# Kernel optimization log

Measured on AMD Instinct MI355X. Metric: run time of the kernel, lower is better.

## Reference

```python
import math
import jax, jax.numpy as jnp
from jax import lax
import numpy as np

D_MODEL, D_STATE, D_CONV, EXPAND = 96, 16, 3, 2
D_INNER = EXPAND * D_MODEL            # 192
DT_RANK = math.ceil(D_MODEL / 16)     # 6
B_, H_, W_ = 2, 64, 64


def setup_inputs() -> dict:
    key = jax.random.key(0)
    ks = jax.random.split(key, 8)
    x = jax.random.normal(ks[0], (B_, H_, W_, D_MODEL), jnp.float32)
    in_proj_w = jax.random.normal(ks[1], (2 * D_INNER, D_MODEL), jnp.float32) * (D_MODEL ** -0.5)
    conv_w = jax.random.normal(ks[2], (D_INNER, 1, D_CONV, D_CONV), jnp.float32) * 0.1  # depthwise OIHW
    conv_b = jax.random.normal(ks[3], (D_INNER,), jnp.float32) * 0.1
    x_proj_weight = jax.random.normal(ks[4], (4, DT_RANK + 2 * D_STATE, D_INNER), jnp.float32) * (D_INNER ** -0.5)
    dt_init_std = DT_RANK ** -0.5
    dt_projs_weight = jax.random.uniform(ks[5], (4, D_INNER, DT_RANK), jnp.float32, -dt_init_std, dt_init_std)
    dt = jnp.exp(jax.random.uniform(ks[6], (4, D_INNER), jnp.float32) * (math.log(0.1) - math.log(0.001)) + math.log(0.001))
    dt = jnp.clip(dt, 1e-4, None)
    dt_projs_bias = dt + jnp.log(-jnp.expm1(-dt))  # inverse softplus init
    A_logs = jnp.log(jnp.tile(jnp.arange(1.0, D_STATE + 1.0, dtype=jnp.float32), (4 * D_INNER, 1)))  # (4*D, N)
    Ds = jnp.ones((4 * D_INNER,), jnp.float32)
    out_norm_w = jnp.ones((D_INNER,), jnp.float32)
    out_norm_b = jnp.zeros((D_INNER,), jnp.float32)
    out_proj_w = jax.random.normal(ks[7], (D_MODEL, D_INNER), jnp.float32) * (D_INNER ** -0.5)
    return dict(x=x, in_proj_w=in_proj_w, conv_w=conv_w, conv_b=conv_b,
                x_proj_weight=x_proj_weight, dt_projs_weight=dt_projs_weight,
                dt_projs_bias=dt_projs_bias, A_logs=A_logs, Ds=Ds,
                out_norm_w=out_norm_w, out_norm_b=out_norm_b, out_proj_w=out_proj_w)


def _ss2d(x, in_proj_w, conv_w, conv_b, x_proj_weight, dt_projs_weight,
          dt_projs_bias, A_logs, Ds, out_norm_w, out_norm_b, out_proj_w):
    B, H, W, C = x.shape
    K = 4
    d_inner = conv_w.shape[0]
    d_state = A_logs.shape[1]
    dt_rank = dt_projs_weight.shape[2]
    L = H * W

    # in_proj + split into x / gate z
    xz = jnp.einsum('bhwc,ec->bhwe', x, in_proj_w)
    xi, z = jnp.split(xz, 2, axis=-1)

    # depthwise 3x3 conv (padding=1) + SiLU, channels-first
    xc = jnp.transpose(xi, (0, 3, 1, 2))  # B,D,H,W
    xc = lax.conv_general_dilated(xc, conv_w, (1, 1), 'SAME',
                                  feature_group_count=d_inner,
                                  dimension_numbers=('NCHW', 'OIHW', 'NCHW'))
    xc = jax.nn.silu(xc + conv_b[None, :, None, None])

    # 4 scan directions: row-major, col-major, and their reverses
    x_hw = xc.reshape(B, d_inner, L)
    x_wh = jnp.transpose(xc, (0, 1, 3, 2)).reshape(B, d_inner, L)
    x_hwwh = jnp.stack([x_hw, x_wh], axis=1)                        # B,2,D,L
    xs = jnp.concatenate([x_hwwh, jnp.flip(x_hwwh, axis=-1)], axis=1)  # B,K,D,L

    x_dbl = jnp.einsum('bkdl,kcd->bkcl', xs, x_proj_weight)
    dts, Bs, Cs = jnp.split(x_dbl, [dt_rank, dt_rank + d_state], axis=2)
    dts = jnp.einsum('bkrl,kdr->bkdl', dts, dt_projs_weight)
    delta = jax.nn.softplus(dts + dt_projs_bias[None, :, :, None])  # B,K,D,L
    A = -jnp.exp(A_logs).reshape(K, d_inner, d_state)               # K,D,N

    # selective scan over L (serial recurrence)
    d_s = jnp.moveaxis(delta, -1, 0)  # L,B,K,D
    u_s = jnp.moveaxis(xs, -1, 0)     # L,B,K,D
    B_s = jnp.moveaxis(Bs, -1, 0)     # L,B,K,N
    C_s = jnp.moveaxis(Cs, -1, 0)     # L,B,K,N

    def step(h, inp):
        d_t, u_t, Bt, Ct = inp
        dA = jnp.exp(d_t[..., None] * A)                       # B,K,D,N
        h = h * dA + (d_t * u_t)[..., None] * Bt[:, :, None, :]
        y = jnp.einsum('bkdn,bkn->bkd', h, Ct)
        return h, y

    h0 = jnp.zeros((B, K, d_inner, d_state), jnp.float32)
    _, ys = lax.scan(step, h0, (d_s, u_s, B_s, C_s))  # ys: L,B,K,D
    ys = jnp.moveaxis(ys, 0, -1)                      # B,K,D,L
    out_y = ys + xs * Ds.reshape(K, d_inner)[None, :, :, None]

    # merge directions back to row-major layout
    inv_y = jnp.flip(out_y[:, 2:4], axis=-1)
    wh_y = jnp.transpose(out_y[:, 1].reshape(B, d_inner, W, H), (0, 1, 3, 2)).reshape(B, d_inner, L)
    invwh_y = jnp.transpose(inv_y[:, 1].reshape(B, d_inner, W, H), (0, 1, 3, 2)).reshape(B, d_inner, L)
    y = out_y[:, 0] + inv_y[:, 0] + wh_y + invwh_y    # B,D,L

    y = jnp.transpose(y, (0, 2, 1)).reshape(B, H, W, d_inner)
    mu = y.mean(-1, keepdims=True)
    var = y.var(-1, keepdims=True)
    y = (y - mu) * lax.rsqrt(var + 1e-5) * out_norm_w + out_norm_b
    y = y * jax.nn.silu(z)
    return jnp.einsum('bhwd,cd->bhwc', y, out_proj_w)


def reference(x, in_proj_w, conv_w, conv_b, x_proj_weight, dt_projs_weight,
              dt_projs_bias, A_logs, Ds, out_norm_w, out_norm_b, out_proj_w):
    return _ss2d(x, in_proj_w, conv_w, conv_b, x_proj_weight, dt_projs_weight,
                 dt_projs_bias, A_logs, Ds, out_norm_w, out_norm_b, out_proj_w)
```

## Files before the change

### kernel.cpp

```cpp
#include <hip/hip_runtime.h>
#include <math.h>

#define DMODEL 96
#define DIN    192
#define NST    16
#define RK     6
#define KDIR   4
#define LLEN   4096
#define BB     2
#define BP_TOT 8192
#define SCH    128
#define TCH    32

typedef float v2f __attribute__((ext_vector_type(2)));

#if __has_builtin(__builtin_elementwise_fma)
__device__ __forceinline__ v2f pk_fma(v2f a, v2f b, v2f c) { return __builtin_elementwise_fma(a, b, c); }
#else
__device__ __forceinline__ v2f pk_fma(v2f a, v2f b, v2f c) { return a * b + c; }
#endif

__global__ __launch_bounds__(192) void k_inproj(const float* __restrict__ x,
                                                const float* __restrict__ Wp,
                                                float* __restrict__ xi,
                                                float* __restrict__ z)
{
    __shared__ float xs[8 * 96];
    const int t  = threadIdx.x;
    const int p0 = blockIdx.x * 8;
    for (int idx = t; idx < 768; idx += 192)
        xs[idx] = x[(size_t)p0 * 96 + idx];
    __syncthreads();

    float acc0[8], acc1[8];
    #pragma unroll
    for (int i = 0; i < 8; ++i) { acc0[i] = 0.f; acc1[i] = 0.f; }
    const float* w0p = Wp + (size_t)t * 96;
    const float* w1p = Wp + (size_t)(t + 192) * 96;
    for (int k = 0; k < 96; k += 4) {
        float4 w0 = *(const float4*)(w0p + k);
        float4 w1 = *(const float4*)(w1p + k);
        #pragma unroll
        for (int p = 0; p < 8; ++p) {
            float4 xv = *(const float4*)&xs[p * 96 + k];
            acc0[p] = fmaf(w0.x, xv.x, fmaf(w0.y, xv.y, fmaf(w0.z, xv.z, fmaf(w0.w, xv.w, acc0[p]))));
            acc1[p] = fmaf(w1.x, xv.x, fmaf(w1.y, xv.y, fmaf(w1.z, xv.z, fmaf(w1.w, xv.w, acc1[p]))));
        }
    }
    #pragma unroll
    for (int p = 0; p < 8; ++p) {
        xi[(size_t)(p0 + p) * 192 + t] = acc0[p];
        z [(size_t)(p0 + p) * 192 + t] = acc1[p];
    }
}

__device__ __forceinline__ int inv_perm(int kd, int p)
{
    if (kd == 0) return p;
    if (kd == 1) return ((p & 63) << 6) | (p >> 6);
    if (kd == 2) return 4095 - p;
    return 4095 - (((p & 63) << 6) | (p >> 6));
}

__device__ __forceinline__ int perm_pos(int k, int l)
{
    if (k == 0) return l;
    if (k == 1) return ((l & 63) << 6) | (l >> 6);
    if (k == 2) return 4095 - l;
    int lr = 4095 - l;
    return ((lr & 63) << 6) | (lr >> 6);
}

__device__ __forceinline__ int perm_dir(int k)
{
    return (k == 0) ? 1 : (k == 1) ? 64 : (k == 2) ? -1 : -64;
}

__device__ __forceinline__ float softplus_fast(float x)
{
    float r = __logf(1.f + __expf(x));
    return (x > 15.f) ? x : r;
}

__device__ __forceinline__ void pow_chain_pk(float e1, v2f* aa)
{
    float e2 = e1 * e1;
    v2f a0; a0.x = e1; a0.y = e2;
    v2f s2; s2.x = e2; s2.y = e2;
    v2f a1 = a0 * s2;
    float e4 = a1.y;
    v2f s4; s4.x = e4; s4.y = e4;
    v2f a2 = a0 * s4;
    v2f a3 = a1 * s4;
    float e8 = a3.y;
    v2f s8; s8.x = e8; s8.y = e8;
    aa[0] = a0; aa[1] = a1; aa[2] = a2; aa[3] = a3;
    aa[4] = a0 * s8;
    aa[5] = a1 * s8;
    aa[6] = a2 * s8;
    aa[7] = a3 * s8;
}

__device__ __forceinline__ float pow_n(float W, int e)
{
    float w2 = W * W, w4 = w2 * w2, w8 = w4 * w4;
    float r = 1.f;
    if (e & 1) r *= W;
    if (e & 2) r *= w2;
    if (e & 4) r *= w4;
    if (e & 8) r *= w8;
    if (e & 16) r = w8 * w8;
    return r;
}

__device__ __forceinline__ int sm_remap(int c)
{
    return (c < 6) ? (32 + c) : (c - 6);
}

__global__ __launch_bounds__(192) void k_convxdbl(const float* __restrict__ xi,
                                                  const float* __restrict__ cw,
                                                  const float* __restrict__ cb,
                                                  const float* __restrict__ xpw,
                                                  float* __restrict__ xc,
                                                  float* __restrict__ xdk)
{
    __shared__ float xs[8 * 192];
    const int t   = threadIdx.x;
    const int p0  = blockIdx.x * 8;
    const int b   = p0 >> 12;
    const int pp0 = p0 & 4095;
    const int row = pp0 >> 6, c0 = pp0 & 63;

    float w9[9];
    #pragma unroll
    for (int i = 0; i < 9; ++i) w9[i] = cw[t * 9 + i];
    const float cbias = cb[t];

    float xv[3][10];
    #pragma unroll
    for (int ky = 0; ky < 3; ++ky) {
        int rr = row + ky - 1;
        #pragma unroll
        for (int kx = 0; kx < 10; ++kx) {
            int cc = c0 + kx - 1;
            float v = 0.f;
            if (rr >= 0 && rr < 64 && cc >= 0 && cc < 64)
                v = xi[((size_t)b * 4096 + rr * 64 + cc) * 192 + t];
            xv[ky][kx] = v;
        }
    }
    #pragma unroll
    for (int p = 0; p < 8; ++p) {
        float s = cbias;
        #pragma unroll
        for (int ky = 0; ky < 3; ++ky)
            #pragma unroll
            for (int kx = 0; kx < 3; ++kx)
                s = fmaf(xv[ky][p + kx], w9[ky * 3 + kx], s);
        float sv = s * (1.f / (1.f + __expf(-s)));
        xc[(size_t)(p0 + p) * 192 + t] = sv;
        xs[p * 192 + t] = sv;
    }
    __syncthreads();
    if (t >= 152) return;

    const int kd = t / 38, r = t % 38;
    float acc[8];
    #pragma unroll
    for (int i = 0; i < 8; ++i) acc[i] = 0.f;
    const float* wr = xpw + (size_t)t * 192;
    for (int k = 0; k < 192; k += 4) {
        float4 w = *(const float4*)(wr + k);
        #pragma unroll
        for (int p = 0; p < 8; ++p) {
            float4 x4 = *(const float4*)&xs[p * 192 + k];
            acc[p] = fmaf(w.x, x4.x, fmaf(w.y, x4.y, fmaf(w.z, x4.z, fmaf(w.w, x4.w, acc[p]))));
        }
    }
    #pragma unroll
    for (int p = 0; p < 8; ++p) {
        int pp = pp0 + p;
        int l  = inv_perm(kd, pp);
        xdk[((size_t)(b * 4 + kd) * 4096 + l) * 38 + r] = acc[p];
    }
}

__global__ __launch_bounds__(192) void k_scan1(const float* __restrict__ xc,
                                               const float* __restrict__ xdk,
                                               const float* __restrict__ dtw,
                                               const float* __restrict__ dtb,
                                               const float* __restrict__ Alog,
                                               float* __restrict__ hend,
                                               float* __restrict__ prodA,
                                               float* __restrict__ Wbuf)
{
    __shared__ float sm[TCH * 40];
    __shared__ float su[TCH * 192];
    const int t   = threadIdx.x;
    const int blk = blockIdx.x;
    const int s = blk & (SCH - 1), k = (blk >> 7) & 3, b = blk >> 9;
    const int kd = k * 192 + t;
    const int l0 = s * TCH;
    const int pstart = perm_pos(k, l0);
    const int dir    = perm_dir(k);

    const float* src = xdk + ((size_t)(b * 4 + k) * 4096 + l0) * 38;
    for (int idx = t; idx < TCH * 38; idx += 192) {
        int st = idx / 38, c = idx % 38;
        sm[st * 40 + sm_remap(c)] = src[idx];
    }
    const float* xcb = xc + (size_t)b * 4096 * 192;
    #pragma unroll
    for (int i = 0; i < TCH; ++i)
        su[i * 192 + t] = xcb[(size_t)(pstart + i * dir) * 192 + t];

    const float A0 = -__expf(Alog[kd * 16]);
    bool fast = true;
    #pragma unroll
    for (int n = 1; n < 16; ++n) {
        float An = -__expf(Alog[kd * 16 + n]);
        fast = fast && (fabsf(An - (float)(n + 1) * A0) <= 1e-3f * fabsf(An));
    }
    float wdt[6];
    #pragma unroll
    for (int r = 0; r < 6; ++r) wdt[r] = dtw[kd * 6 + r];
    const float bias = dtb[kd];

    __syncthreads();

    size_t base = (size_t)blk * 3072 + t * 16;

    if (fast) {
        v2f h2[8];
        #pragma unroll
        for (int i = 0; i < 8; ++i) { h2[i].x = 0.f; h2[i].y = 0.f; }
        float cd = 0.f;
        for (int st = 0; st < TCH; ++st) {
            const float* r = &sm[st * 40];
            float u = su[st * 192 + t];
            float4 dq = *(const float4*)(r + 32);
            float xv = bias + dq.x * wdt[0] + dq.y * wdt[1] + dq.z * wdt[2]
                            + dq.w * wdt[3] + r[36] * wdt[4] + r[37] * wdt[5];
            float delta = softplus_fast(xv);
            cd += delta;
            float du = delta * u;
            v2f du2; du2.x = du; du2.y = du;
            v2f aa2[8];
            pow_chain_pk(__expf(delta * A0), aa2);
            const v2f* rb = (const v2f*)r;
            #pragma unroll
            for (int i = 0; i < 8; ++i)
                h2[i] = pk_fma(h2[i], aa2[i], du2 * rb[i]);
        }
        Wbuf[(size_t)blk * 192 + t] = __expf(cd * A0);
        #pragma unroll
        for (int i = 0; i < 4; ++i)
            *(float4*)&hend[base + 4 * i] =
                make_float4(h2[2*i].x, h2[2*i].y, h2[2*i+1].x, h2[2*i+1].y);
    } else {
        float h[16];
        #pragma unroll
        for (int n = 0; n < 16; ++n) h[n] = 0.f;
        float cd = 0.f;
        for (int st = 0; st < TCH; ++st) {
            const float* r = &sm[st * 40];
            float u = su[st * 192 + t];
            float xv = bias;
            #pragma unroll
            for (int j = 0; j < 6; ++j) xv += r[32 + j] * wdt[j];
            float delta = softplus_fast(xv);
            cd += delta;
            float du = delta * u;
            #pragma unroll
            for (int n = 0; n < 16; ++n) {
                float An = -__expf(Alog[kd * 16 + n]);
                h[n] = fmaf(h[n], __expf(delta * An), du * r[n]);
            }
        }
        #pragma unroll
        for (int n = 0; n < 16; ++n)
            prodA[base + n] = __expf(-__expf(Alog[kd * 16 + n]) * cd);
        #pragma unroll
        for (int i = 0; i < 4; ++i)
            *(float4*)&hend[base + 4 * i] = make_float4(h[4*i], h[4*i+1], h[4*i+2], h[4*i+3]);
    }
}

__global__ __launch_bounds__(256) void k_scan2(const float* __restrict__ hend,
                                               float* __restrict__ prodA,
                                               const float* __restrict__ Wbuf,
                                               const float* __restrict__ Alog)
{
    __shared__ float smA[256], smH[256];
    const int t = threadIdx.x;
    const int g = t >> 4, n = t & 15;
    const int bk = blockIdx.x / 192, d = blockIdx.x % 192;
    const int kd = (bk & 3) * 192 + d;
    const size_t base = (size_t)bk * SCH * 3072 + d * 16 + n;

    const float A0 = -__expf(Alog[kd * 16]);
    bool fast = true;
    #pragma unroll
    for (int m = 1; m < 16; ++m) {
        float An = -__expf(Alog[kd * 16 + m]);
        fast = fast && (fabsf(An - (float)(m + 1) * A0) <= 1e-3f * fabsf(An));
    }

    float a_[8], h_[8];
    float A = 1.f, H = 0.f;
    #pragma unroll
    for (int i = 0; i < 8; ++i) {
        int s = g * 8 + i;
        size_t rec = base + (size_t)s * 3072;
        float ai;
        if (fast) {
            float W = Wbuf[((size_t)bk * SCH + s) * 192 + d];
            ai = pow_n(W, n + 1);
        } else {
            ai = prodA[rec];
        }
        a_[i] = ai;
        h_[i] = hend[rec];
        H = fmaf(ai, H, h_[i]);
        A *= ai;
    }
    smA[t] = A; smH[t] = H;
    __syncthreads();
    if (t < 16) {
        float carry = 0.f;
        for (int g2 = 0; g2 < 16; ++g2) {
            float ta = smA[g2 * 16 + t], th = smH[g2 * 16 + t];
            smH[g2 * 16 + t] = carry;
            carry = fmaf(ta, carry, th);
        }
    }
    __syncthreads();
    float carry = smH[t];
    #pragma unroll
    for (int i = 0; i < 8; ++i) {
        size_t rec = base + (size_t)(g * 8 + i) * 3072;
        prodA[rec] = carry;
        carry = fmaf(a_[i], carry, h_[i]);
    }
}

__global__ __launch_bounds__(192) void k_scan3(const float* __restrict__ xc,
                                               const float* __restrict__ xdk,
                                               const float* __restrict__ dtw,
                                               const float* __restrict__ dtb,
                                               const float* __restrict__ Alog,
                                               const float* __restrict__ Ds,
                                               const float* __restrict__ hinit,
                                               float* __restrict__ yk)
{
    __shared__ float sm[TCH * 40];
    __shared__ float su[TCH * 192];
    const int t   = threadIdx.x;
    const int blk = blockIdx.x;
    const int s = blk & (SCH - 1), k = (blk >> 7) & 3, b = blk >> 9;
    const int kd = k * 192 + t;
    const int l0 = s * TCH;
    const int pstart = perm_pos(k, l0);
    const int dir    = perm_dir(k);

    const float* src = xdk + ((size_t)(b * 4 + k) * 4096 + l0) * 38;
    for (int idx = t; idx < TCH * 38; idx += 192) {
        int st = idx / 38, c = idx % 38;
        sm[st * 40 + sm_remap(c)] = src[idx];
    }
    const float* xcb = xc + (size_t)b * 4096 * 192;
    #pragma unroll
    for (int i = 0; i < TCH; ++i)
        su[i * 192 + t] = xcb[(size_t)(pstart + i * dir) * 192 + t];

    const float A0 = -__expf(Alog[kd * 16]);
    bool fast = true;
    #pragma unroll
    for (int n = 1; n < 16; ++n) {
        float An = -__expf(Alog[kd * 16 + n]);
        fast = fast && (fabsf(An - (float)(n + 1) * A0) <= 1e-3f * fabsf(An));
    }
    float wdt[6];
    #pragma unroll
    for (int r = 0; r < 6; ++r) wdt[r] = dtw[kd * 6 + r];
    const float bias = dtb[kd];
    const float Dk   = Ds[kd];

    size_t hbase = (size_t)blk * 3072 + t * 16;
    float* yp = yk + (size_t)(b * 4 + k) * 4096 * 192 + (size_t)pstart * 192 + t;
    const int ystep = dir * 192;

    __syncthreads();

    if (fast) {
        v2f h2[8];
        #pragma unroll
        for (int i = 0; i < 4; ++i) {
            float4 v = *(const float4*)&hinit[hbase + 4 * i];
            h2[2*i].x = v.x; h2[2*i].y = v.y; h2[2*i+1].x = v.z; h2[2*i+1].y = v.w;
        }
        for (int st = 0; st < TCH; ++st) {
            const float* r = &sm[st * 40];
            float u = su[st * 192 + t];
            float4 dq = *(const float4*)(r + 32);
            float xv = bias + dq.x * wdt[0] + dq.y * wdt[1] + dq.z * wdt[2]
                            + dq.w * wdt[3] + r[36] * wdt[4] + r[37] * wdt[5];
            float delta = softplus_fast(xv);
            float du = delta * u;
            v2f du2; du2.x = du; du2.y = du;
            v2f aa2[8];
            pow_chain_pk(__expf(delta * A0), aa2);
            const v2f* rb = (const v2f*)r;
            const v2f* rc = (const v2f*)(r + 16);
            v2f acc2; acc2.x = Dk * u; acc2.y = 0.f;
            #pragma unroll
            for (int i = 0; i < 8; ++i) {
                h2[i] = pk_fma(h2[i], aa2[i], du2 * rb[i]);
                acc2  = pk_fma(h2[i], rc[i], acc2);
            }
            *yp = acc2.x + acc2.y;
            yp += ystep;
        }
    } else {
        float h[16];
        #pragma unroll
        for (int i = 0; i < 4; ++i) {
            float4 v = *(const float4*)&hinit[hbase + 4 * i];
            h[4*i] = v.x; h[4*i+1] = v.y; h[4*i+2] = v.z; h[4*i+3] = v.w;
        }
        for (int st = 0; st < TCH; ++st) {
            const float* r = &sm[st * 40];
            float u = su[st * 192 + t];
            float xv = bias;
            #pragma unroll
            for (int j = 0; j < 6; ++j) xv += r[32 + j] * wdt[j];
            float delta = softplus_fast(xv);
            float du = delta * u;
            float acc = Dk * u;
            #pragma unroll
            for (int n = 0; n < 16; ++n) {
                float An = -__expf(Alog[kd * 16 + n]);
                h[n] = fmaf(h[n], __expf(delta * An), du * r[n]);
                acc  = fmaf(h[n], r[16 + n], acc);
            }
            *yp = acc;
            yp += ystep;
        }
    }
}

__global__ __launch_bounds__(192) void k_lnout(const float* __restrict__ yk,
                                               const float* __restrict__ zb,
                                               const float* __restrict__ onw,
                                               const float* __restrict__ onb,
                                               const float* __restrict__ Wo,
                                               float* __restrict__ out)
{
    __shared__ float ys[1536];
    __shared__ float ps[192], pq[192];
    __shared__ float mu[8], ri[8];
    const int t   = threadIdx.x;
    const int p0  = blockIdx.x * 8;
    const int b   = p0 >> 12;
    const int pp0 = p0 & 4095;
    const size_t KSTR = (size_t)4096 * 192;

    #pragma unroll
    for (int i = 0; i < 8; ++i) {
        size_t base = ((size_t)(b * 4) * 4096 + pp0 + i) * 192 + t;
        ys[i * 192 + t] = yk[base] + yk[base + KSTR] + yk[base + 2 * KSTR] + yk[base + 3 * KSTR];
    }
    __syncthreads();

    {
        int pg = t / 24, j = t % 24;
        float s1 = 0.f, s2 = 0.f;
        #pragma unroll
        for (int m = 0; m < 8; ++m) {
            float v = ys[pg * 192 + j + 24 * m];
            s1 += v; s2 += v * v;
        }
        ps[t] = s1; pq[t] = s2;
    }
    __syncthreads();
    if (t < 8) {
        float s1 = 0.f, s2 = 0.f;
        #pragma unroll
        for (int j = 0; j < 24; ++j) { s1 += ps[t * 24 + j]; s2 += pq[t * 24 + j]; }
        float mean = s1 * (1.f / 192.f);
        float var  = s2 * (1.f / 192.f) - mean * mean;
        mu[t] = mean;
        ri[t] = rsqrtf(var + 1e-5f);
    }
    __syncthreads();

    {
        float w = onw[t], bo = onb[t];
        #pragma unroll
        for (int i = 0; i < 8; ++i) {
            float v  = ys[i * 192 + t];
            float yn = (v - mu[i]) * ri[i] * w + bo;
            float zv = zb[(size_t)(p0 + i) * 192 + t];
            float sg = 1.f / (1.f + __expf(-zv));
            ys[i * 192 + t] = yn * (zv * sg);
        }
    }
    __syncthreads();

    const int pg = t / 96, c = t % 96;
    float acc[4];
    #pragma unroll
    for (int i = 0; i < 4; ++i) acc[i] = 0.f;
    const float* wr = Wo + (size_t)c * 192;
    for (int k = 0; k < 192; k += 4) {
        float4 w = *(const float4*)(wr + k);
        #pragma unroll
        for (int i = 0; i < 4; ++i) {
            float4 xv = *(const float4*)&ys[(pg * 4 + i) * 192 + k];
            acc[i] = fmaf(w.x, xv.x, fmaf(w.y, xv.y, fmaf(w.z, xv.z, fmaf(w.w, xv.w, acc[i]))));
        }
    }
    #pragma unroll
    for (int i = 0; i < 4; ++i)
        out[(size_t)(p0 + pg * 4 + i) * 96 + c] = acc[i];
}

extern "C" void kernel_launch(void* const* d_in, const int* in_sizes, int n_in,
                              void* d_out, int out_size, void* d_ws, size_t ws_size,
                              hipStream_t stream)
{
    const float* x    = (const float*)d_in[0];
    const float* Wp   = (const float*)d_in[1];
    const float* cw   = (const float*)d_in[2];
    const float* cb   = (const float*)d_in[3];
    const float* xpw  = (const float*)d_in[4];
    const float* dtw  = (const float*)d_in[5];
    const float* dtb  = (const float*)d_in[6];
    const float* Alog = (const float*)d_in[7];
    const float* Ds   = (const float*)d_in[8];
    const float* onw  = (const float*)d_in[9];
    const float* onb  = (const float*)d_in[10];
    const float* Wo   = (const float*)d_in[11];
    float* out = (float*)d_out;

    const size_t NBP  = (size_t)BP_TOT * 192;
    const size_t NXD  = (size_t)BB * 4 * 4096 * 38;
    const size_t NSC  = (size_t)BB * 4 * SCH * 3072;
    const size_t NW   = (size_t)BB * 4 * SCH * 192;
    float* WS    = (float*)d_ws;
    float* xibuf = WS;
    float* zb    = WS + NBP;
    float* xc    = WS + 2 * NBP;
    float* xdk   = WS + 3 * NBP;
    float* hend  = xdk + NXD;
    float* prodA = hend + NSC;
    float* Wbuf  = prodA + NSC;
    float* yk    = Wbuf + NW;

    k_inproj  <<<1024, 192, 0, stream>>>(x, Wp, xibuf, zb);
    k_convxdbl<<<1024, 192, 0, stream>>>(xibuf, cw, cb, xpw, xc, xdk);
    k_scan1   <<<1024, 192, 0, stream>>>(xc, xdk, dtw, dtb, Alog, hend, prodA, Wbuf);
    k_scan2   <<<1536, 256, 0, stream>>>(hend, prodA, Wbuf, Alog);
    k_scan3   <<<1024, 192, 0, stream>>>(xc, xdk, dtw, dtb, Alog, Ds, prodA, yk);
    k_lnout   <<<1024, 192, 0, stream>>>(yk, zb, onw, onb, Wo, out);
}
```

Baseline: 200.3 us.

## Fuse in_proj into depthwise conv kernel by recomputing halo projections

Merges the in_proj kernel into the conv/x_proj kernel. Each block now loads a 3x10 halo of raw input pixels into shared memory and recomputes the xi projection for all 30 halo positions, rather than reading xi back from global memory. This removes one kernel launch and the xi buffer round trip. The cost is about 3.75x redundant xi matmul work, 30 accumulator registers, and extra shared memory.

Measured after the change: 226.5 us. 1.13x slower.

```diff
diff --git a/kernel.cpp b/kernel.cpp
--- a/kernel.cpp
+++ b/kernel.cpp
@@ -19,40 +19,6 @@
 #else
 __device__ __forceinline__ v2f pk_fma(v2f a, v2f b, v2f c) { return a * b + c; }
 #endif
-
-__global__ __launch_bounds__(192) void k_inproj(const float* __restrict__ x,
-                                                const float* __restrict__ Wp,
-                                                float* __restrict__ xi,
-                                                float* __restrict__ z)
-{
-    __shared__ float xs[8 * 96];
-    const int t  = threadIdx.x;
-    const int p0 = blockIdx.x * 8;
-    for (int idx = t; idx < 768; idx += 192)
-        xs[idx] = x[(size_t)p0 * 96 + idx];
-    __syncthreads();
-
-    float acc0[8], acc1[8];
-    #pragma unroll
-    for (int i = 0; i < 8; ++i) { acc0[i] = 0.f; acc1[i] = 0.f; }
-    const float* w0p = Wp + (size_t)t * 96;
-    const float* w1p = Wp + (size_t)(t + 192) * 96;
-    for (int k = 0; k < 96; k += 4) {
-        float4 w0 = *(const float4*)(w0p + k);
-        float4 w1 = *(const float4*)(w1p + k);
-        #pragma unroll
-        for (int p = 0; p < 8; ++p) {
-            float4 xv = *(const float4*)&xs[p * 96 + k];
-            acc0[p] = fmaf(w0.x, xv.x, fmaf(w0.y, xv.y, fmaf(w0.z, xv.z, fmaf(w0.w, xv.w, acc0[p]))));
-            acc1[p] = fmaf(w1.x, xv.x, fmaf(w1.y, xv.y, fmaf(w1.z, xv.z, fmaf(w1.w, xv.w, acc1[p]))));
-        }
-    }
-    #pragma unroll
-    for (int p = 0; p < 8; ++p) {
-        xi[(size_t)(p0 + p) * 192 + t] = acc0[p];
-        z [(size_t)(p0 + p) * 192 + t] = acc1[p];
-    }
-}
 
 __device__ __forceinline__ int inv_perm(int kd, int p)
 {
@@ -118,13 +84,16 @@
     return (c < 6) ? (32 + c) : (c - 6);
 }
 
-__global__ __launch_bounds__(192) void k_convxdbl(const float* __restrict__ xi,
-                                                  const float* __restrict__ cw,
-                                                  const float* __restrict__ cb,
-                                                  const float* __restrict__ xpw,
-                                                  float* __restrict__ xc,
-                                                  float* __restrict__ xdk)
-{
+__global__ __launch_bounds__(192) void k_fused(const float* __restrict__ x,
+                                               const float* __restrict__ Wp,
+                                               const float* __restrict__ cw,
+                                               const float* __restrict__ cb,
+                                               const float* __restrict__ xpw,
+                                               float* __restrict__ z,
+                                               float* __restrict__ xc,
+                                               float* __restrict__ xdk)
+{
+    __shared__ float xh[30 * 96];
     __shared__ float xs[8 * 192];
     const int t   = threadIdx.x;
     const int p0  = blockIdx.x * 8;
@@ -132,24 +101,43 @@
     const int pp0 = p0 & 4095;
     const int row = pp0 >> 6, c0 = pp0 & 63;
 
+    for (int idx = t; idx < 2880; idx += 192) {
+        int hp = idx / 96, kk = idx - hp * 96;
+        int rr = row + hp / 10 - 1;
+        int cc = c0 + hp % 10 - 1;
+        float v = 0.f;
+        if (rr >= 0 && rr < 64 && cc >= 0 && cc < 64)
+            v = x[((size_t)b * 4096 + rr * 64 + cc) * 96 + kk];
+        xh[idx] = v;
+    }
+    __syncthreads();
+
+    float acc[30], accz[8];
+    #pragma unroll
+    for (int i = 0; i < 30; ++i) acc[i] = 0.f;
+    #pragma unroll
+    for (int i = 0; i < 8; ++i) accz[i] = 0.f;
+    const float* w0p = Wp + (size_t)t * 96;
+    const float* w1p = Wp + (size_t)(t + 192) * 96;
+    for (int k = 0; k < 96; k += 4) {
+        float4 w0 = *(const float4*)(w0p + k);
+        float4 w1 = *(const float4*)(w1p + k);
+        #pragma unroll
+        for (int hp = 0; hp < 30; ++hp) {
+            float4 xv = *(const float4*)&xh[hp * 96 + k];
+            acc[hp] = fmaf(w0.x, xv.x, fmaf(w0.y, xv.y, fmaf(w0.z, xv.z, fmaf(w0.w, xv.w, acc[hp]))));
+        }
+        #pragma unroll
+        for (int p = 0; p < 8; ++p) {
+            float4 xv = *(const float4*)&xh[(11 + p) * 96 + k];
+            accz[p] = fmaf(w1.x, xv.x, fmaf(w1.y, xv.y, fmaf(w1.z, xv.z, fmaf(w1.w, xv.w, accz[p]))));
+        }
+    }
+
     float w9[9];
     #pragma unroll
     for (int i = 0; i < 9; ++i) w9[i] = cw[t * 9 + i];
     const float cbias = cb[t];
-
-    float xv[3][10];
-    #pragma unroll
-    for (int ky = 0; ky < 3; ++ky) {
-        int rr = row + ky - 1;
-        #pragma unroll
-        for (int kx = 0; kx < 10; ++kx) {
-            int cc = c0 + kx - 1;
-            float v = 0.f;
-            if (rr >= 0 && rr < 64 && cc >= 0 && cc < 64)
-                v = xi[((size_t)b * 4096 + rr * 64 + cc) * 192 + t];
-            xv[ky][kx] = v;
-        }
-    }
     #pragma unroll
     for (int p = 0; p < 8; ++p) {
         float s = cbias;
@@ -157,32 +145,33 @@
         for (int ky = 0; ky < 3; ++ky)
             #pragma unroll
             for (int kx = 0; kx < 3; ++kx)
-                s = fmaf(xv[ky][p + kx], w9[ky * 3 + kx], s);
+                s = fmaf(acc[ky * 10 + p + kx], w9[ky * 3 + kx], s);
         float sv = s * (1.f / (1.f + __expf(-s)));
         xc[(size_t)(p0 + p) * 192 + t] = sv;
         xs[p * 192 + t] = sv;
+        z[(size_t)(p0 + p) * 192 + t] = accz[p];
     }
     __syncthreads();
     if (t >= 152) return;
 
     const int kd = t / 38, r = t % 38;
-    float acc[8];
-    #pragma unroll
-    for (int i = 0; i < 8; ++i) acc[i] = 0.f;
+    float pacc[8];
+    #pragma unroll
+    for (int i = 0; i < 8; ++i) pacc[i] = 0.f;
     const float* wr = xpw + (size_t)t * 192;
     for (int k = 0; k < 192; k += 4) {
         float4 w = *(const float4*)(wr + k);
         #pragma unroll
         for (int p = 0; p < 8; ++p) {
             float4 x4 = *(const float4*)&xs[p * 192 + k];
-            acc[p] = fmaf(w.x, x4.x, fmaf(w.y, x4.y, fmaf(w.z, x4.z, fmaf(w.w, x4.w, acc[p]))));
+            pacc[p] = fmaf(w.x, x4.x, fmaf(w.y, x4.y, fmaf(w.z, x4.z, fmaf(w.w, x4.w, pacc[p]))));
         }
     }
     #pragma unroll
     for (int p = 0; p < 8; ++p) {
         int pp = pp0 + p;
         int l  = inv_perm(kd, pp);
-        xdk[((size_t)(b * 4 + kd) * 4096 + l) * 38 + r] = acc[p];
+        xdk[((size_t)(b * 4 + kd) * 4096 + l) * 38 + r] = pacc[p];
     }
 }
 
@@ -549,19 +538,17 @@
     const size_t NSC  = (size_t)BB * 4 * SCH * 3072;
     const size_t NW   = (size_t)BB * 4 * SCH * 192;
     float* WS    = (float*)d_ws;
-    float* xibuf = WS;
-    float* zb    = WS + NBP;
-    float* xc    = WS + 2 * NBP;
-    float* xdk   = WS + 3 * NBP;
+    float* zb    = WS;
+    float* xc    = WS + NBP;
+    float* xdk   = WS + 2 * NBP;
     float* hend  = xdk + NXD;
     float* prodA = hend + NSC;
     float* Wbuf  = prodA + NSC;
     float* yk    = Wbuf + NW;
 
-    k_inproj  <<<1024, 192, 0, stream>>>(x, Wp, xibuf, zb);
-    k_convxdbl<<<1024, 192, 0, stream>>>(xibuf, cw, cb, xpw, xc, xdk);
-    k_scan1   <<<1024, 192, 0, stream>>>(xc, xdk, dtw, dtb, Alog, hend, prodA, Wbuf);
-    k_scan2   <<<1536, 256, 0, stream>>>(hend, prodA, Wbuf, Alog);
-    k_scan3   <<<1024, 192, 0, stream>>>(xc, xdk, dtw, dtb, Alog, Ds, prodA, yk);
-    k_lnout   <<<1024, 192, 0, stream>>>(yk, zb, onw, onb, Wo, out);
-}
+    k_fused <<<1024, 192, 0, stream>>>(x, Wp, cw, cb, xpw, zb, xc, xdk);
+    k_scan1 <<<1024, 192, 0, stream>>>(xc, xdk, dtw, dtb, Alog, hend, prodA, Wbuf);
+    k_scan2 <<<1536, 256, 0, stream>>>(hend, prodA, Wbuf, Alog);
+    k_scan3 <<<1024, 192, 0, stream>>>(xc, xdk, dtw, dtb, Alog, Ds, prodA, yk);
+    k_lnout <<<1024, 192, 0, stream>>>(yk, zb, onw, onb, Wo, out);
+}
```
